# Optimization experiments

Measured on AMD Instinct MI355X. Metric: run time of the kernel, lower is better.

## Reference

```python
import jax, jax.numpy as jnp
import numpy as np

B, T, C, H = 8, 2048, 1024, 64

def setup_inputs() -> dict:
    key = jax.random.key(0)
    kx, kq, kk, kv = jax.random.split(key, 4)
    scale = 1.0 / np.sqrt(C)
    return {
        "x": jax.random.normal(kx, (B, T, C), dtype=jnp.float32),
        "Wq": jax.random.normal(kq, (C, H), dtype=jnp.float32) * scale,
        "Wk": jax.random.normal(kk, (C, H), dtype=jnp.float32) * scale,
        "Wv": jax.random.normal(kv, (C, H), dtype=jnp.float32) * scale,
    }

def reference(x, Wq, Wk, Wv):
    # q,k,v: [B,T,H]
    q = jnp.einsum('btc,ch->bth', x, Wq)
    k = jnp.einsum('btc,ch->bth', x, Wk)
    v = jnp.einsum('btc,ch->bth', x, Wv)
    scale = k.shape[-1] ** -0.5
    wei = jnp.einsum('bth,bsh->bts', q, k) * scale  # [B,T,T]
    causal = jnp.tril(jnp.ones((x.shape[1], x.shape[1]), dtype=bool))
    wei = jnp.where(causal, wei, -jnp.inf)
    wei = jax.nn.softmax(wei, axis=-1)
    out = jnp.einsum('bts,bsh->bth', wei, v)  # [B,T,H]
    return out
```

## Files before the change

kernel.cpp:

```cpp
#include <hip/hip_runtime.h>

#define B_ 8
#define T_ 2048
#define C_ 1024
#define H_ 64

typedef __bf16 bf16x8 __attribute__((ext_vector_type(8)));
typedef float  f32x4  __attribute__((ext_vector_type(4)));
typedef unsigned short u16x8 __attribute__((ext_vector_type(8)));

__device__ __forceinline__ unsigned short f2bf(float f) {
    unsigned u = __builtin_bit_cast(unsigned, f);
    u += 0x8000u;
    return (unsigned short)(u >> 16);
}

__device__ __forceinline__ float bf2f(unsigned short v) {
    unsigned u = ((unsigned)v) << 16;
    return __builtin_bit_cast(float, u);
}

__device__ __forceinline__ unsigned pack2(float lo, float hi) {
    unsigned a = __builtin_bit_cast(unsigned, lo) + 0x8000u;
    unsigned b = __builtin_bit_cast(unsigned, hi) + 0x8000u;
    return (a >> 16) | (b & 0xffff0000u);
}

union U8 { unsigned u32[4]; u16x8 v; };

__device__ __forceinline__ u16x8 cvt8(float4 f0, float4 f1) {
    U8 r;
    r.u32[0] = pack2(f0.x, f0.y);
    r.u32[1] = pack2(f0.z, f0.w);
    r.u32[2] = pack2(f1.x, f1.y);
    r.u32[3] = pack2(f1.z, f1.w);
    return r.v;
}

__device__ __forceinline__ bf16x8 load8_bf(const unsigned short* p) {
    return __builtin_bit_cast(bf16x8, *(const u16x8*)p);
}

__device__ __forceinline__ void gload_lds16(const float* g, float* l) {
    __builtin_amdgcn_global_load_lds(
        (const __attribute__((address_space(1))) unsigned int*)g,
        (__attribute__((address_space(3))) unsigned int*)l, 16, 0, 0);
}


__global__ void cast_weights(const float* __restrict__ Wq,
                             const float* __restrict__ Wk,
                             const float* __restrict__ Wv,
                             unsigned short* __restrict__ Wtf) {
    int idx = blockIdx.x * blockDim.x + threadIdx.x;
    int n   = idx % 192;
    int c   = idx / 192;
    int w   = n >> 6;
    int h   = n & 63;
    const float* W = (w == 0) ? Wq : (w == 1) ? Wk : Wv;
    int nt = n >> 4, l16 = n & 15;
    int kk = c >> 5, quad = (c >> 3) & 3, j = c & 7;
    Wtf[(size_t)(nt * 32 + kk) * 512 + l16 * 32 + quad * 8 + j] =
        f2bf(W[(size_t)c * H_ + h]);
}

#define NCH 16

__global__ __launch_bounds__(512, 2) void qkv_proj(
        const float* __restrict__ x,
        const unsigned short* __restrict__ Wtf,
        unsigned short* __restrict__ Qf,
        unsigned short* __restrict__ Kf,
        unsigned short* __restrict__ Vf) {
    __shared__ __attribute__((aligned(16))) char smem[163840];
    unsigned short* E = (unsigned short*)smem;

    const int tid   = threadIdx.x;
    const int w     = tid >> 6;
    const int strip = w & 3;
    const int nh    = w >> 2;
    const int lane  = tid & 63;
    const int l16   = lane & 15;
    const int quad  = lane >> 4;
    const size_t rblk = (size_t)blockIdx.x * 64;
    const int bb    = (int)(rblk >> 11);
    const int tloc0 = (int)(rblk & (T_ - 1));
    const int t16_0 = tloc0 >> 4;
    const int s32_0 = tloc0 >> 5;
    const int xsw   = l16 & 7;
    const int bs8   = (((l16 * 4 + quad) ^ (l16 >> 1)) * 8);

    auto stage = [&](int c) {
        float* Ab          = (float*)(smem + (c & 3) * 16384);
        char*  Bb          = smem + 65536 + (c & 3) * 24576;
#pragma unroll
        for (int q = 0; q < 5; q++) {
            int j = w * 5 + q;
            if (j < 16) {
                int row  = j * 4 + (lane >> 4);
                int slot = lane & 15;
                int g    = slot ^ (row & 7);
                gload_lds16(x + (rblk + row) * C_ + c * 64 + g * 4,
                            Ab + j * 256);
            } else {
                int jb = j - 16;
                int nt = jb >> 1, kkl = jb & 1;
                int sl = lane ^ (lane >> 3);
                gload_lds16(
                    (const float*)(Wtf + ((size_t)nt * 32 + c * 2 + kkl) * 512
                                   + (size_t)sl * 8),
                    (float*)(Bb + jb * 1024));
            }
        }
    };

    f32x4 acc[6];
#pragma unroll
    for (int i = 0; i < 6; i++) acc[i] = (f32x4){0.f, 0.f, 0.f, 0.f};

    stage(0); stage(1); stage(2);

    for (int c = 0; c < NCH; c++) {
        if (c < NCH - 2)       asm volatile("s_waitcnt vmcnt(10)" ::: "memory");
        else if (c == NCH - 2) asm volatile("s_waitcnt vmcnt(5)"  ::: "memory");
        else                   asm volatile("s_waitcnt vmcnt(0)"  ::: "memory");
        __builtin_amdgcn_s_barrier();
        __builtin_amdgcn_sched_barrier(0);

        if (c + 3 < NCH) stage(c + 3);

        const float* Ab = (const float*)(smem + (c & 3) * 16384)
                          + (strip * 16 + l16) * 64;
        const unsigned short* Bb =
            (const unsigned short*)(smem + 65536 + (c & 3) * 24576);
#pragma unroll
        for (int kk = 0; kk < 2; kk++) {
            int g0 = kk * 8 + quad * 2;
            float4 f0 = *(const float4*)(Ab + ((g0    ) ^ xsw) * 4);
            float4 f1 = *(const float4*)(Ab + ((g0 + 1) ^ xsw) * 4);
            bf16x8 a0 = __builtin_bit_cast(bf16x8, cvt8(f0, f1));
#pragma unroll
            for (int i = 0; i < 6; i++) {
                bf16x8 b = load8_bf(Bb + ((nh * 6 + i) * 2 + kk) * 512 + bs8);
                acc[i] = __builtin_amdgcn_mfma_f32_16x16x32_bf16(a0, b, acc[i], 0, 0, 0);
            }
        }
    }

    {
        const int g   = strip >> 1;
        const int st2 = strip & 1;
        unsigned short* Eg = E + g * 6144;
#pragma unroll
        for (int i = 0; i < 6; i++) {
            int nt = nh * 6 + i;
#pragma unroll
            for (int r = 0; r < 4; r++) {
                unsigned short bv = f2bf(acc[i][r]);
                int off;
                if (nt < 4) {
                    off = (st2 * 2 + (nt >> 1)) * 512 +
                          (quad * 4 + r) * 32 + (nt & 1) * 16 + l16;
                } else if (nt < 8) {
                    int nk = nt - 4;
                    off = 2048 + (st2 * 2 + (nk >> 1)) * 512 +
                          (quad * 4 + r) * 32 + (nk & 1) * 16 + l16;
                } else {
                    int ht = nt - 8;
                    off = 4096 + ht * 512 + l16 * 32 + st2 * 16 + quad * 4 + r;
                }
                Eg[off] = bv;
            }
        }
    }
    __syncthreads();

#pragma unroll
    for (int c3 = 0; c3 < 3; c3++) {
        int gi  = c3 * 512 + tid;
        int grp = (gi >= 768) ? 1 : 0;
        int wi  = gi - grp * 768;
        int ch  = wi >> 6;
        int gg  = wi & 63;
        const unsigned short* src = E + grp * 6144 + ch * 512 + gg * 8;
        int t16g = t16_0 + grp * 2;
        int s32g = s32_0 + grp;
        unsigned short* dst;
        if (ch < 4) {
            dst = Qf + ((size_t)(bb * 128 + t16g + (ch >> 1)) * 2 + (ch & 1)) * 512;
        } else if (ch < 8) {
            int c2 = ch - 4;
            dst = Kf + ((size_t)(bb * 128 + t16g + (c2 >> 1)) * 2 + (c2 & 1)) * 512;
        } else {
            dst = Vf + ((size_t)(bb * 64 + s32g) * 4 + (ch - 8)) * 512;
        }
        *(u16x8*)(dst + gg * 8) = *(const u16x8*)src;
    }
}

#define PROW 33
#define OMS2 66

__global__ __launch_bounds__(512) void attn(
        const unsigned short* __restrict__ Qf,
        const unsigned short* __restrict__ Kf,
        const unsigned short* __restrict__ Vf,
        float* __restrict__ out) {
    __shared__ unsigned int ps_[8 * 32 * PROW];
    __shared__ unsigned short Om_[8 * 32 * OMS2];
    __shared__ float mred_[8][32];
    __shared__ float lred_[8][32];

    const int tid  = threadIdx.x;
    const int wave = tid >> 6;
    const int half = wave >> 2;
    const int wv4  = wave & 3;
    const int lane = tid & 63;
    const int l16  = lane & 15;
    const int quad = lane >> 4;
    const int b    = blockIdx.x & 7;
    const int jp   = blockIdx.x >> 3;
    const int qt32 = half ? (63 - jp) : jp;
    const int q0   = qt32 * 32;
    const int tdiag = qt32 >> 1;

    const int loff = l16 * 32 + quad * 8;

    bf16x8 qf[2][2];
#pragma unroll
    for (int qg = 0; qg < 2; qg++) {
        const unsigned short* Qfb = Qf + (size_t)((b * 128 + qt32 * 2 + qg) * 2) * 512;
        qf[qg][0] = load8_bf(Qfb + loff);
        qf[qg][1] = load8_bf(Qfb + 512 + loff);
    }

    f32x4 o[8];
#pragma unroll
    for (int i = 0; i < 8; i++) o[i] = (f32x4){0.f, 0.f, 0.f, 0.f};
    float m_run[2] = {-1e30f, -1e30f}, l_run[2] = {0.f, 0.f};

    const float scale = 0.125f;
    const unsigned short* Kfb = Kf + (size_t)b * 128 * 1024;
    const unsigned short* Vfb = Vf + (size_t)b * 64 * 2048;
    unsigned int* Pw = &ps_[wave * 32 * PROW];

    for (int t = wv4; t <= tdiag; t += 4) {
        bf16x8 vf[8];
#pragma unroll
        for (int ks = 0; ks < 2; ks++)
#pragma unroll
            for (int ht = 0; ht < 4; ht++)
                vf[ht * 2 + ks] = load8_bf(
                    Vfb + ((size_t)(t * 2 + ks) * 4 + ht) * 512 + loff);

        f32x4 s[2][4];
#pragma unroll
        for (int nt = 0; nt < 4; nt++) {
            const unsigned short* kp = Kfb + (size_t)(t * 4 + nt) * 1024;
            bf16x8 kf0 = load8_bf(kp + loff);
            bf16x8 kf1 = load8_bf(kp + 512 + loff);
#pragma unroll
            for (int qg = 0; qg < 2; qg++) {
                f32x4 z = (f32x4){0.f, 0.f, 0.f, 0.f};
                z = __builtin_amdgcn_mfma_f32_16x16x32_bf16(kf0, qf[qg][0], z, 0, 0, 0);
                z = __builtin_amdgcn_mfma_f32_16x16x32_bf16(kf1, qf[qg][1], z, 0, 0, 0);
                s[qg][nt] = z;
            }
        }

#pragma unroll
        for (int qg = 0; qg < 2; qg++)
#pragma unroll
            for (int nt = 0; nt < 4; nt++)
#pragma unroll
                for (int r = 0; r < 4; r++) s[qg][nt][r] *= scale;

        if (t == tdiag) {
#pragma unroll
            for (int qg = 0; qg < 2; qg++) {
                int q = q0 + qg * 16 + l16;
#pragma unroll
                for (int nt = 0; nt < 4; nt++)
#pragma unroll
                    for (int r = 0; r < 4; r++) {
                        int key = t * 64 + nt * 16 + quad * 4 + r;
                        if (key > q) s[qg][nt][r] = -1e30f;
                    }
            }
        }

#pragma unroll
        for (int qg = 0; qg < 2; qg++) {
            float m0 = fmaxf(fmaxf(s[qg][0][0], s[qg][0][1]), fmaxf(s[qg][0][2], s[qg][0][3]));
            float m1 = fmaxf(fmaxf(s[qg][1][0], s[qg][1][1]), fmaxf(s[qg][1][2], s[qg][1][3]));
            float m2 = fmaxf(fmaxf(s[qg][2][0], s[qg][2][1]), fmaxf(s[qg][2][2], s[qg][2][3]));
            float m3 = fmaxf(fmaxf(s[qg][3][0], s[qg][3][1]), fmaxf(s[qg][3][2], s[qg][3][3]));
            float mx = fmaxf(fmaxf(m0, m1), fmaxf(m2, m3));
            mx = fmaxf(mx, __shfl_xor(mx, 16));
            mx = fmaxf(mx, __shfl_xor(mx, 32));
            const float m_new = fmaxf(m_run[qg], mx);
            const float alpha = __expf(m_run[qg] - m_new);
            m_run[qg] = m_new;

            float rs = 0.f;
#pragma unroll
            for (int nt = 0; nt < 4; nt++) {
#pragma unroll
                for (int i = 0; i < 2; i++) {
                    float p0 = __expf(s[qg][nt][2 * i]     - m_new);
                    float p1 = __expf(s[qg][nt][2 * i + 1] - m_new);
                    rs += p0 + p1;
                    Pw[(qg * 16 + l16) * PROW + nt * 8 + quad * 2 + i] = pack2(p0, p1);
                }
            }
            rs += __shfl_xor(rs, 16);
            rs += __shfl_xor(rs, 32);
            l_run[qg] = l_run[qg] * alpha + rs;

#pragma unroll
            for (int ht = 0; ht < 4; ht++)
#pragma unroll
                for (int r = 0; r < 4; r++) o[qg * 4 + ht][r] *= alpha;
        }

#pragma unroll
        for (int ks = 0; ks < 2; ks++) {
#pragma unroll
            for (int qg = 0; qg < 2; qg++) {
                bf16x8 pB = __builtin_bit_cast(bf16x8,
                    *(const u16x8*)(&Pw[(qg * 16 + l16) * PROW + ks * 16 + quad * 4]));
#pragma unroll
                for (int ht = 0; ht < 4; ht++)
                    o[qg * 4 + ht] = __builtin_amdgcn_mfma_f32_16x16x32_bf16(
                        vf[ht * 2 + ks], pB, o[qg * 4 + ht], 0, 0, 0);
            }
        }
    }

#pragma unroll
    for (int qg = 0; qg < 2; qg++) {
#pragma unroll
        for (int ht = 0; ht < 4; ht++)
#pragma unroll
            for (int r = 0; r < 4; r++)
                Om_[(wave * 32 + qg * 16 + l16) * OMS2 + ht * 16 + quad * 4 + r] =
                    f2bf(o[qg * 4 + ht][r]);
        if (quad == 0) {
            mred_[wave][qg * 16 + l16] = m_run[qg];
            lred_[wave][qg * 16 + l16] = l_run[qg];
        }
    }
    __syncthreads();

    const int half2 = tid >> 8;
    const int t2    = tid & 255;
    const int hcol  = t2 & 63;
    const int qr0   = t2 >> 6;
    const int qt32f = half2 ? (63 - jp) : jp;
    const int q0f   = qt32f * 32;
#pragma unroll
    for (int qq = 0; qq < 8; qq++) {
        const int q = qr0 + qq * 4;
        float M = -1e30f;
#pragma unroll
        for (int w = 0; w < 4; w++) M = fmaxf(M, mred_[half2 * 4 + w][q]);
        float lt = 0.f, ov = 0.f;
#pragma unroll
        for (int w = 0; w < 4; w++) {
            float e = __expf(mred_[half2 * 4 + w][q] - M);
            lt += e * lred_[half2 * 4 + w][q];
            ov += e * bf2f(Om_[((half2 * 4 + w) * 32 + q) * OMS2 + hcol]);
        }
        out[((size_t)b * T_ + q0f + q) * H_ + hcol] = ov / lt;
    }
}

extern "C" void kernel_launch(void* const* d_in, const int* in_sizes, int n_in,
                              void* d_out, int out_size, void* d_ws, size_t ws_size,
                              hipStream_t stream) {
    const float* x  = (const float*)d_in[0];
    const float* Wq = (const float*)d_in[1];
    const float* Wk = (const float*)d_in[2];
    const float* Wv = (const float*)d_in[3];
    float* out = (float*)d_out;

    unsigned short* Qf  = (unsigned short*)d_ws;
    unsigned short* Kf  = Qf + (size_t)B_ * T_ * H_;
    unsigned short* Vf  = Kf + (size_t)B_ * T_ * H_;
    unsigned short* Wtf = Vf + (size_t)B_ * T_ * H_;

    cast_weights<<<(192 * C_) / 256, 256, 0, stream>>>(Wq, Wk, Wv, Wtf);
    qkv_proj<<<B_ * T_ / 64, 512, 0, stream>>>(x, Wtf, Qf, Kf, Vf);
    attn<<<B_ * (T_ / 64), 512, 0, stream>>>(Qf, Kf, Vf, out);
}
```

Measured before the change: 138.0 us.

## Shrink qkv_proj blocks to 32 rows and use double-buffered staging

The projection kernel now handles 32 rows per block with 256 threads instead of 64 rows with 512, which doubles the grid and cuts shared memory from 160KB to 64KB. The triple-buffered async pipeline with hand-tuned vmcnt waits becomes a simple double buffer with __syncthreads per chunk. The goal is better occupancy and more blocks to spread across CUs. In exchange, each block reloads the full weight tile for fewer rows, and the plain barrier scheme exposes more load latency.

```diff
diff --git a/kernel.cpp b/kernel.cpp
--- a/kernel.cpp
+++ b/kernel.cpp
@@ -66,23 +66,23 @@
 
 #define NCH 16
 
-__global__ __launch_bounds__(512, 2) void qkv_proj(
+__global__ __launch_bounds__(256, 2) void qkv_proj(
         const float* __restrict__ x,
         const unsigned short* __restrict__ Wtf,
         unsigned short* __restrict__ Qf,
         unsigned short* __restrict__ Kf,
         unsigned short* __restrict__ Vf) {
-    __shared__ __attribute__((aligned(16))) char smem[163840];
+    __shared__ __attribute__((aligned(16))) char smem[65536];
     unsigned short* E = (unsigned short*)smem;
 
     const int tid   = threadIdx.x;
     const int w     = tid >> 6;
-    const int strip = w & 3;
-    const int nh    = w >> 2;
+    const int strip = w & 1;
+    const int nh    = w >> 1;
     const int lane  = tid & 63;
     const int l16   = lane & 15;
     const int quad  = lane >> 4;
-    const size_t rblk = (size_t)blockIdx.x * 64;
+    const size_t rblk = (size_t)blockIdx.x * 32;
     const int bb    = (int)(rblk >> 11);
     const int tloc0 = (int)(rblk & (T_ - 1));
     const int t16_0 = tloc0 >> 4;
@@ -91,19 +91,19 @@
     const int bs8   = (((l16 * 4 + quad) ^ (l16 >> 1)) * 8);
 
     auto stage = [&](int c) {
-        float* Ab          = (float*)(smem + (c & 3) * 16384);
-        char*  Bb          = smem + 65536 + (c & 3) * 24576;
-#pragma unroll
-        for (int q = 0; q < 5; q++) {
-            int j = w * 5 + q;
-            if (j < 16) {
+        float* Ab = (float*)(smem + (c & 1) * 8192);
+        char*  Bb = smem + 16384 + (c & 1) * 24576;
+#pragma unroll
+        for (int q = 0; q < 8; q++) {
+            int j = w * 8 + q;
+            if (j < 8) {
                 int row  = j * 4 + (lane >> 4);
                 int slot = lane & 15;
                 int g    = slot ^ (row & 7);
                 gload_lds16(x + (rblk + row) * C_ + c * 64 + g * 4,
                             Ab + j * 256);
             } else {
-                int jb = j - 16;
+                int jb = j - 8;
                 int nt = jb >> 1, kkl = jb & 1;
                 int sl = lane ^ (lane >> 3);
                 gload_lds16(
@@ -118,21 +118,16 @@
 #pragma unroll
     for (int i = 0; i < 6; i++) acc[i] = (f32x4){0.f, 0.f, 0.f, 0.f};
 
-    stage(0); stage(1); stage(2);
+    stage(0);
+    __syncthreads();
 
     for (int c = 0; c < NCH; c++) {
-        if (c < NCH - 2)       asm volatile("s_waitcnt vmcnt(10)" ::: "memory");
-        else if (c == NCH - 2) asm volatile("s_waitcnt vmcnt(5)"  ::: "memory");
-        else                   asm volatile("s_waitcnt vmcnt(0)"  ::: "memory");
-        __builtin_amdgcn_s_barrier();
-        __builtin_amdgcn_sched_barrier(0);
-
-        if (c + 3 < NCH) stage(c + 3);
-
-        const float* Ab = (const float*)(smem + (c & 3) * 16384)
+        if (c < NCH - 1) stage(c + 1);
+
+        const float* Ab = (const float*)(smem + (c & 1) * 8192)
                           + (strip * 16 + l16) * 64;
         const unsigned short* Bb =
-            (const unsigned short*)(smem + 65536 + (c & 3) * 24576);
+            (const unsigned short*)(smem + 16384 + (c & 1) * 24576);
 #pragma unroll
         for (int kk = 0; kk < 2; kk++) {
             int g0 = kk * 8 + quad * 2;
@@ -145,56 +140,47 @@
                 acc[i] = __builtin_amdgcn_mfma_f32_16x16x32_bf16(a0, b, acc[i], 0, 0, 0);
             }
         }
-    }
-
-    {
-        const int g   = strip >> 1;
-        const int st2 = strip & 1;
-        unsigned short* Eg = E + g * 6144;
-#pragma unroll
-        for (int i = 0; i < 6; i++) {
-            int nt = nh * 6 + i;
-#pragma unroll
-            for (int r = 0; r < 4; r++) {
-                unsigned short bv = f2bf(acc[i][r]);
-                int off;
-                if (nt < 4) {
-                    off = (st2 * 2 + (nt >> 1)) * 512 +
-                          (quad * 4 + r) * 32 + (nt & 1) * 16 + l16;
-                } else if (nt < 8) {
-                    int nk = nt - 4;
-                    off = 2048 + (st2 * 2 + (nk >> 1)) * 512 +
-                          (quad * 4 + r) * 32 + (nk & 1) * 16 + l16;
-                } else {
-                    int ht = nt - 8;
-                    off = 4096 + ht * 512 + l16 * 32 + st2 * 16 + quad * 4 + r;
-                }
-                Eg[off] = bv;
-            }
+        __syncthreads();
+    }
+
+#pragma unroll
+    for (int i = 0; i < 6; i++) {
+        int nt = nh * 6 + i;
+#pragma unroll
+        for (int r = 0; r < 4; r++) {
+            unsigned short bv = f2bf(acc[i][r]);
+            int off;
+            if (nt < 4) {
+                off = (strip * 2 + (nt >> 1)) * 512 +
+                      (quad * 4 + r) * 32 + (nt & 1) * 16 + l16;
+            } else if (nt < 8) {
+                int nk = nt - 4;
+                off = 2048 + (strip * 2 + (nk >> 1)) * 512 +
+                      (quad * 4 + r) * 32 + (nk & 1) * 16 + l16;
+            } else {
+                int ht = nt - 8;
+                off = 4096 + ht * 512 + l16 * 32 + strip * 16 + quad * 4 + r;
+            }
+            E[off] = bv;
         }
     }
     __syncthreads();
 
 #pragma unroll
     for (int c3 = 0; c3 < 3; c3++) {
-        int gi  = c3 * 512 + tid;
-        int grp = (gi >= 768) ? 1 : 0;
-        int wi  = gi - grp * 768;
-        int ch  = wi >> 6;
-        int gg  = wi & 63;
-        const unsigned short* src = E + grp * 6144 + ch * 512 + gg * 8;
-        int t16g = t16_0 + grp * 2;
-        int s32g = s32_0 + grp;
+        int gi = c3 * 256 + tid;
+        int ch = gi >> 6;
+        int g  = gi & 63;
         unsigned short* dst;
         if (ch < 4) {
-            dst = Qf + ((size_t)(bb * 128 + t16g + (ch >> 1)) * 2 + (ch & 1)) * 512;
+            dst = Qf + ((size_t)(bb * 128 + t16_0 + (ch >> 1)) * 2 + (ch & 1)) * 512;
         } else if (ch < 8) {
             int c2 = ch - 4;
-            dst = Kf + ((size_t)(bb * 128 + t16g + (c2 >> 1)) * 2 + (c2 & 1)) * 512;
+            dst = Kf + ((size_t)(bb * 128 + t16_0 + (c2 >> 1)) * 2 + (c2 & 1)) * 512;
         } else {
-            dst = Vf + ((size_t)(bb * 64 + s32g) * 4 + (ch - 8)) * 512;
-        }
-        *(u16x8*)(dst + gg * 8) = *(const u16x8*)src;
+            dst = Vf + ((size_t)(bb * 64 + s32_0) * 4 + (ch - 8)) * 512;
+        }
+        *(u16x8*)(dst + g * 8) = *(const u16x8*)(&E[ch * 512 + g * 8]);
     }
 }
 
@@ -390,6 +376,6 @@
     unsigned short* Wtf = Vf + (size_t)B_ * T_ * H_;
 
     cast_weights<<<(192 * C_) / 256, 256, 0, stream>>>(Wq, Wk, Wv, Wtf);
-    qkv_proj<<<B_ * T_ / 64, 512, 0, stream>>>(x, Wtf, Qf, Kf, Vf);
+    qkv_proj<<<B_ * T_ / 32, 256, 0, stream>>>(x, Wtf, Qf, Kf, Vf);
     attn<<<B_ * (T_ / 64), 512, 0, stream>>>(Qf, Kf, Vf, out);
 }
```

After: 136.8 us. Within noise of the previous version (-0.9%).
